# Kernel optimization log

Measured on AMD Instinct MI355X. Metric: run time of the kernel, lower is better.

## Reference

```python
import jax, jax.numpy as jnp
import numpy as np
import math

B, N, D, H, PAIR = 4, 512, 512, 16, 64
DH = D // H

def setup_inputs() -> dict:
    key = jax.random.key(0)
    ks = jax.random.split(key, 8)
    x = jax.random.normal(ks[0], (B, N, D), dtype=jnp.float32)
    pair_bias = jax.random.normal(ks[1], (B, N, N, PAIR), dtype=jnp.float32)
    atom_mask = jax.random.randint(ks[2], (B, N), 0, 2).astype(jnp.bool_)
    s = 1.0 / math.sqrt(D)
    Wq = jax.random.normal(ks[3], (D, D), dtype=jnp.float32) * s
    Wk = jax.random.normal(ks[4], (D, D), dtype=jnp.float32) * s
    Wv = jax.random.normal(ks[5], (D, D), dtype=jnp.float32) * s
    Wo = jax.random.normal(ks[6], (D, D), dtype=jnp.float32) * s
    Wp = jax.random.normal(ks[7], (PAIR, H), dtype=jnp.float32) * (1.0 / math.sqrt(PAIR))
    return {"x": x, "pair_bias": pair_bias, "Wq": Wq, "Wk": Wk, "Wv": Wv,
            "Wo": Wo, "Wp": Wp, "atom_mask": atom_mask}

def reference(x, pair_bias, Wq, Wk, Wv, Wo, Wp, atom_mask):
    b, n, d = x.shape
    # projections -> [B, H, N, DH]
    q = (x @ Wq).reshape(b, n, H, DH).transpose(0, 2, 1, 3)
    k = (x @ Wk).reshape(b, n, H, DH).transpose(0, 2, 1, 3)
    v = (x @ Wv).reshape(b, n, H, DH).transpose(0, 2, 1, 3)
    scores = jnp.einsum('bhnd,bhmd->bhnm', q, k) / math.sqrt(DH)
    # pair bias projected to heads: [B, H, N, N]
    bias = jnp.einsum('bnmp,ph->bhnm', pair_bias, Wp)
    pair_mask = atom_mask[:, :, None] & atom_mask[:, None, :]        # [B, N, N]
    bias = jnp.where(pair_mask[:, None, :, :], bias, 0.0)
    scores = scores + bias
    # key masking with finite large negative, as in the original
    scores = jnp.where(atom_mask[:, None, None, :], scores, jnp.float32(-1e6))
    attn = jax.nn.softmax(scores, axis=-1)
    out = jnp.einsum('bhnm,bhmd->bhnd', attn, v)
    out = out.transpose(0, 2, 1, 3).reshape(b, n, d)
    final = out @ Wo
    final = jnp.where(atom_mask[:, :, None], final, 0.0)
    return (final, attn)
```

## Files before the change

kernel.cpp:

```cpp
#include <hip/hip_runtime.h>

typedef __attribute__((ext_vector_type(8))) short short8;
typedef __attribute__((ext_vector_type(4))) float f32x4;

#define NB 4
#define NN 512
#define ND 512
#define NH 16
#define NDH 32
#define NPAIR 64

static __device__ __forceinline__ unsigned short f2bf(float f) {
    union { float f; unsigned int i; } x; x.f = f;
    unsigned int i = x.i;
    unsigned int r = (i + 0x7fffu + ((i >> 16) & 1u)) >> 16;
    return (unsigned short)r;
}

static __device__ __forceinline__ short8 cvt8(const float4 lo, const float4 hi) {
    short8 r;
    r[0] = (short)f2bf(lo.x); r[1] = (short)f2bf(lo.y);
    r[2] = (short)f2bf(lo.z); r[3] = (short)f2bf(lo.w);
    r[4] = (short)f2bf(hi.x); r[5] = (short)f2bf(hi.y);
    r[6] = (short)f2bf(hi.z); r[7] = (short)f2bf(hi.w);
    return r;
}

__global__ __launch_bounds__(256) void qkv_kernel(
    const float* __restrict__ x, const float* __restrict__ Wq,
    const float* __restrict__ Wk, const float* __restrict__ Wv,
    float* __restrict__ q_ws, float* __restrict__ k_ws, ushort* __restrict__ vT_ws)
{
    __shared__ float xs[8 * 512];
    const int tid = threadIdx.x;
    const int row0 = blockIdx.x * 8;
    const int which = blockIdx.y;
    const float* W = (which == 0) ? Wq : (which == 1) ? Wk : Wv;

    {
        const float4* xg = (const float4*)(x + row0 * 512);
        float4* s = (float4*)xs;
        #pragma unroll
        for (int i = 0; i < 4; ++i) s[tid + i * 256] = xg[tid + i * 256];
    }
    __syncthreads();

    const int c0 = tid * 2;
    float acc[8][2];
    #pragma unroll
    for (int r = 0; r < 8; ++r) { acc[r][0] = 0.f; acc[r][1] = 0.f; }

    for (int kk = 0; kk < 512; kk += 4) {
        float w[4][2];
        #pragma unroll
        for (int j = 0; j < 4; ++j) {
            const float2 u = *(const float2*)(W + (kk + j) * 512 + c0);
            w[j][0] = u.x; w[j][1] = u.y;
        }
        #pragma unroll
        for (int r = 0; r < 8; ++r) {
            const float4 xv = *(const float4*)(xs + r * 512 + kk);
            acc[r][0] = fmaf(xv.x, w[0][0], acc[r][0]);
            acc[r][1] = fmaf(xv.x, w[0][1], acc[r][1]);
            acc[r][0] = fmaf(xv.y, w[1][0], acc[r][0]);
            acc[r][1] = fmaf(xv.y, w[1][1], acc[r][1]);
            acc[r][0] = fmaf(xv.z, w[2][0], acc[r][0]);
            acc[r][1] = fmaf(xv.z, w[2][1], acc[r][1]);
            acc[r][0] = fmaf(xv.w, w[3][0], acc[r][0]);
            acc[r][1] = fmaf(xv.w, w[3][1], acc[r][1]);
        }
    }

    const int h = c0 >> 5, dh = c0 & 31;
    #pragma unroll
    for (int r = 0; r < 8; ++r) {
        int row = row0 + r, b = row >> 9, n = row & 511;
        if (which < 2) {
            float* dst = (which == 0 ? q_ws : k_ws) + (((b * 16 + h) * 512 + n) * 32 + dh);
            *(float2*)dst = make_float2(acc[r][0], acc[r][1]);
        } else {
            ushort* base = vT_ws + ((b * 16 + h) * 32 + dh) * 512 + n;
            base[0]   = f2bf(acc[r][0]);
            base[512] = f2bf(acc[r][1]);
        }
    }
}

__global__ __launch_bounds__(256) void bias_kernel(
    const float* __restrict__ pb, const float* __restrict__ Wp,
    float* __restrict__ bias_out)
{
    const int tid = threadIdx.x;
    const int lane = tid & 63, wid = tid >> 6;
    const int col = lane & 15, quad = lane >> 4;

    short8 b0, b1;
    #pragma unroll
    for (int j = 0; j < 8; ++j) {
        b0[j] = (short)f2bf(Wp[(quad * 8 + j) * 16 + col]);
        b1[j] = (short)f2bf(Wp[(32 + quad * 8 + j) * 16 + col]);
    }

    const int gw = blockIdx.x * 4 + wid;
    #pragma unroll
    for (int i = 0; i < 8; ++i) {
        int tile = gw * 8 + i;
        int mt = tile & 31, n = (tile >> 5) & 511, b = tile >> 14;
        int m0 = mt * 16;
        const float* ap = pb + ((size_t)((b * 512 + n) * 512) + m0 + col) * 64 + quad * 8;
        short8 a0 = cvt8(*(const float4*)(ap),      *(const float4*)(ap + 4));
        short8 a1 = cvt8(*(const float4*)(ap + 32), *(const float4*)(ap + 36));
        f32x4 acc = {0.f, 0.f, 0.f, 0.f};
        acc = __builtin_amdgcn_mfma_f32_16x16x32_bf16(a0, b0, acc, 0, 0, 0);
        acc = __builtin_amdgcn_mfma_f32_16x16x32_bf16(a1, b1, acc, 0, 0, 0);
        float4 o = make_float4(acc[0], acc[1], acc[2], acc[3]);
        *(float4*)(bias_out + ((size_t)(b * 16 + col) * 512 + n) * 512 + m0 + quad * 4) = o;
    }
}

__global__ __launch_bounds__(256) void attn_kernel(
    const float* __restrict__ q_ws, const float* __restrict__ k_ws,
    const int* __restrict__ am, float* __restrict__ attn)
{
    __shared__ float qs[32 * 32];
    __shared__ int amq[32];
    __shared__ float wred[8];
    const int tid = threadIdx.x, lane = tid & 63, wid = tid >> 6;
    const int bh = blockIdx.x >> 4, nt = blockIdx.x & 15;
    const int b = bh >> 4;
    const int n0 = nt * 32;

    {
        const float4* qg = (const float4*)(q_ws + (size_t)(bh * 512 + n0) * 32);
        ((float4*)qs)[tid] = qg[tid];
    }
    if (tid < 32) amq[tid] = am[b * 512 + n0 + tid];

    float k0[32], k1[32];
    {
        const float4* kp  = (const float4*)(k_ws + (size_t)(bh * 512 + tid) * 32);
        const float4* kp2 = (const float4*)(k_ws + (size_t)(bh * 512 + tid + 256) * 32);
        #pragma unroll
        for (int j = 0; j < 8; ++j) {
            float4 u = kp[j];
            k0[j * 4 + 0] = u.x; k0[j * 4 + 1] = u.y; k0[j * 4 + 2] = u.z; k0[j * 4 + 3] = u.w;
            float4 u2 = kp2[j];
            k1[j * 4 + 0] = u2.x; k1[j * 4 + 1] = u2.y; k1[j * 4 + 2] = u2.z; k1[j * 4 + 3] = u2.w;
        }
    }
    const int km0 = am[b * 512 + tid];
    const int km1 = am[b * 512 + 256 + tid];
    __syncthreads();

    const float scale = 0.17677669529663687f;
    float* arow = attn + (size_t)(bh * 512 + n0) * 512;

    for (int r = 0; r < 32; ++r) {
        float s0 = 0.f, s1 = 0.f;
        const float4* q4 = (const float4*)(qs + r * 32);
        #pragma unroll
        for (int j = 0; j < 8; ++j) {
            float4 qv = q4[j];
            s0 = fmaf(qv.x, k0[j * 4 + 0], s0); s1 = fmaf(qv.x, k1[j * 4 + 0], s1);
            s0 = fmaf(qv.y, k0[j * 4 + 1], s0); s1 = fmaf(qv.y, k1[j * 4 + 1], s1);
            s0 = fmaf(qv.z, k0[j * 4 + 2], s0); s1 = fmaf(qv.z, k1[j * 4 + 2], s1);
            s0 = fmaf(qv.w, k0[j * 4 + 3], s0); s1 = fmaf(qv.w, k1[j * 4 + 3], s1);
        }
        float bias0 = arow[r * 512 + tid];
        float bias1 = arow[r * 512 + tid + 256];
        int rm = amq[r];
        s0 = s0 * scale + ((rm && km0) ? bias0 : 0.f);
        s1 = s1 * scale + ((rm && km1) ? bias1 : 0.f);
        if (!km0) s0 = -1e6f;
        if (!km1) s1 = -1e6f;

        float mloc = fmaxf(s0, s1);
        #pragma unroll
        for (int off = 32; off > 0; off >>= 1) mloc = fmaxf(mloc, __shfl_xor(mloc, off));
        if (lane == 0) wred[wid] = mloc;
        __syncthreads();
        float mx = fmaxf(fmaxf(wred[0], wred[1]), fmaxf(wred[2], wred[3]));
        float p0 = __expf(s0 - mx), p1 = __expf(s1 - mx);
        float sl = p0 + p1;
        #pragma unroll
        for (int off = 32; off > 0; off >>= 1) sl += __shfl_xor(sl, off);
        if (lane == 0) wred[4 + wid] = sl;
        __syncthreads();
        float inv = 1.0f / (wred[4] + wred[5] + wred[6] + wred[7]);
        arow[r * 512 + tid]       = p0 * inv;
        arow[r * 512 + tid + 256] = p1 * inv;
        __syncthreads();
    }
}

__global__ __launch_bounds__(256) void av_kernel(
    const float* __restrict__ attn, const ushort* __restrict__ vT,
    float* __restrict__ out_ws)
{
    const int tid = threadIdx.x, lane = tid & 63, wid = tid >> 6;
    const int col = lane & 15, quad = lane >> 4;
    const int wt = blockIdx.x * 4 + wid;
    const int rt = wt & 31, bh = wt >> 5;
    const int n0 = rt * 16;

    const float*  ap  = attn + (size_t)(bh * 512 + n0 + col) * 512 + quad * 8;
    const ushort* vp0 = vT + (size_t)(bh * 32 + col) * 512 + quad * 8;
    const ushort* vp1 = vp0 + 16 * 512;

    f32x4 acc0 = {0.f, 0.f, 0.f, 0.f}, acc1 = {0.f, 0.f, 0.f, 0.f};
    #pragma unroll 4
    for (int kc = 0; kc < 16; ++kc) {
        int mo = kc * 32;
        short8 a  = cvt8(*(const float4*)(ap + mo), *(const float4*)(ap + mo + 4));
        short8 v0 = *(const short8*)(vp0 + mo);
        short8 v1 = *(const short8*)(vp1 + mo);
        acc0 = __builtin_amdgcn_mfma_f32_16x16x32_bf16(a, v0, acc0, 0, 0, 0);
        acc1 = __builtin_amdgcn_mfma_f32_16x16x32_bf16(a, v1, acc1, 0, 0, 0);
    }
    const int b = bh >> 4, h = bh & 15;
    float* op = out_ws + (size_t)(b * 512 + n0 + quad * 4) * 512 + h * 32;
    #pragma unroll
    for (int r = 0; r < 4; ++r) {
        op[r * 512 + col]      = acc0[r];
        op[r * 512 + 16 + col] = acc1[r];
    }
}

__global__ __launch_bounds__(256) void out_kernel(
    const float* __restrict__ out_in, const float* __restrict__ Wo,
    const int* __restrict__ am, float* __restrict__ fin)
{
    __shared__ float xs[8 * 512];
    const int tid = threadIdx.x;
    const int row0 = blockIdx.x * 8;
    {
        const float4* g = (const float4*)(out_in + (size_t)row0 * 512);
        float4* s = (float4*)xs;
        #pragma unroll
        for (int i = 0; i < 4; ++i) s[tid + i * 256] = g[tid + i * 256];
    }
    __syncthreads();

    const int c0 = tid * 2;
    float acc[8][2];
    #pragma unroll
    for (int r = 0; r < 8; ++r) { acc[r][0] = 0.f; acc[r][1] = 0.f; }

    for (int kk = 0; kk < 512; kk += 4) {
        float w[4][2];
        #pragma unroll
        for (int j = 0; j < 4; ++j) {
            const float2 u = *(const float2*)(Wo + (kk + j) * 512 + c0);
            w[j][0] = u.x; w[j][1] = u.y;
        }
        #pragma unroll
        for (int r = 0; r < 8; ++r) {
            const float4 xv = *(const float4*)(xs + r * 512 + kk);
            acc[r][0] = fmaf(xv.x, w[0][0], acc[r][0]);
            acc[r][1] = fmaf(xv.x, w[0][1], acc[r][1]);
            acc[r][0] = fmaf(xv.y, w[1][0], acc[r][0]);
            acc[r][1] = fmaf(xv.y, w[1][1], acc[r][1]);
            acc[r][0] = fmaf(xv.z, w[2][0], acc[r][0]);
            acc[r][1] = fmaf(xv.z, w[2][1], acc[r][1]);
            acc[r][0] = fmaf(xv.w, w[3][0], acc[r][0]);
            acc[r][1] = fmaf(xv.w, w[3][1], acc[r][1]);
        }
    }
    #pragma unroll
    for (int r = 0; r < 8; ++r) {
        int row = row0 + r, b = row >> 9, n = row & 511;
        float msk = am[b * 512 + n] ? 1.0f : 0.0f;
        *(float2*)(fin + (size_t)row * 512 + c0) =
            make_float2(acc[r][0] * msk, acc[r][1] * msk);
    }
}

extern "C" void kernel_launch(void* const* d_in, const int* in_sizes, int n_in,
                              void* d_out, int out_size, void* d_ws, size_t ws_size,
                              hipStream_t stream)
{
    const float* x  = (const float*)d_in[0];
    const float* pb = (const float*)d_in[1];
    const float* Wq = (const float*)d_in[2];
    const float* Wk = (const float*)d_in[3];
    const float* Wv = (const float*)d_in[4];
    const float* Wo = (const float*)d_in[5];
    const float* Wp = (const float*)d_in[6];
    const int*   am = (const int*)d_in[7];

    float* fin  = (float*)d_out;
    float* attn = fin + (size_t)NB * NN * ND;

    float*  q_ws   = (float*)d_ws;
    float*  k_ws   = (float*)((char*)d_ws + 4u * 1024 * 1024);
    ushort* vT     = (ushort*)((char*)d_ws + 8u * 1024 * 1024);
    float*  out_ws = (float*)((char*)d_ws + 10u * 1024 * 1024);

    hipLaunchKernelGGL(qkv_kernel, dim3(256, 3), dim3(256), 0, stream,
                       x, Wq, Wk, Wv, q_ws, k_ws, vT);
    hipLaunchKernelGGL(bias_kernel, dim3(2048), dim3(256), 0, stream,
                       pb, Wp, attn);
    hipLaunchKernelGGL(attn_kernel, dim3(1024), dim3(256), 0, stream,
                       q_ws, k_ws, am, attn);
    hipLaunchKernelGGL(av_kernel, dim3(512), dim3(256), 0, stream,
                       attn, vT, out_ws);
    hipLaunchKernelGGL(out_kernel, dim3(256), dim3(256), 0, stream,
                       out_ws, Wo, am, fin);
}
```

Measured before the change: 601.2 us.

## Fuse softmax with AV matmul, store pair bias as bf16 workspace

The pair-bias projection now writes to a separate bf16 workspace instead of an fp32 staging copy inside the attn output. The softmax kernel and the attention-times-V kernel are merged, so each block computes AV for its 32 rows right after writing them, with the key dimension split across waves and partial sums reduced in shared memory. Double-buffered reduction slots remove one barrier per row. This cuts bias write and read traffic and one kernel launch, and lets the attn re-read hit cache, at the cost of bf16 rounding of the bias and lower AV parallelism per block.

```diff
diff --git a/kernel.cpp b/kernel.cpp
--- a/kernel.cpp
+++ b/kernel.cpp
@@ -10,13 +10,15 @@
 #define NDH 32
 #define NPAIR 64
 
+static __device__ __forceinline__ float bf2f(unsigned short u) {
+    union { unsigned int i; float f; } x; x.i = ((unsigned int)u) << 16; return x.f;
+}
 static __device__ __forceinline__ unsigned short f2bf(float f) {
     union { float f; unsigned int i; } x; x.f = f;
     unsigned int i = x.i;
     unsigned int r = (i + 0x7fffu + ((i >> 16) & 1u)) >> 16;
     return (unsigned short)r;
 }
-
 static __device__ __forceinline__ short8 cvt8(const float4 lo, const float4 hi) {
     short8 r;
     r[0] = (short)f2bf(lo.x); r[1] = (short)f2bf(lo.y);
@@ -88,7 +90,7 @@
 
 __global__ __launch_bounds__(256) void bias_kernel(
     const float* __restrict__ pb, const float* __restrict__ Wp,
-    float* __restrict__ bias_out)
+    ushort* __restrict__ bias_ws)
 {
     const int tid = threadIdx.x;
     const int lane = tid & 63, wid = tid >> 6;
@@ -113,21 +115,25 @@
         f32x4 acc = {0.f, 0.f, 0.f, 0.f};
         acc = __builtin_amdgcn_mfma_f32_16x16x32_bf16(a0, b0, acc, 0, 0, 0);
         acc = __builtin_amdgcn_mfma_f32_16x16x32_bf16(a1, b1, acc, 0, 0, 0);
-        float4 o = make_float4(acc[0], acc[1], acc[2], acc[3]);
-        *(float4*)(bias_out + ((size_t)(b * 16 + col) * 512 + n) * 512 + m0 + quad * 4) = o;
-    }
-}
-
-__global__ __launch_bounds__(256) void attn_kernel(
+        ushort4 o;
+        o.x = f2bf(acc[0]); o.y = f2bf(acc[1]); o.z = f2bf(acc[2]); o.w = f2bf(acc[3]);
+        *(ushort4*)(bias_ws + ((size_t)(b * 16 + col) * 512 + n) * 512 + m0 + quad * 4) = o;
+    }
+}
+
+__global__ __launch_bounds__(256) void attn_av_kernel(
     const float* __restrict__ q_ws, const float* __restrict__ k_ws,
-    const int* __restrict__ am, float* __restrict__ attn)
+    const ushort* __restrict__ bias_ws, const ushort* __restrict__ vT,
+    const int* __restrict__ am, float* __restrict__ attn,
+    float* __restrict__ out_ws)
 {
     __shared__ float qs[32 * 32];
     __shared__ int amq[32];
-    __shared__ float wred[8];
+    __shared__ float wred[2][2][4];
+    __shared__ float red[4 * 528];
     const int tid = threadIdx.x, lane = tid & 63, wid = tid >> 6;
     const int bh = blockIdx.x >> 4, nt = blockIdx.x & 15;
-    const int b = bh >> 4;
+    const int b = bh >> 4, h = bh & 15;
     const int n0 = nt * 32;
 
     {
@@ -154,6 +160,7 @@
 
     const float scale = 0.17677669529663687f;
     float* arow = attn + (size_t)(bh * 512 + n0) * 512;
+    const ushort* brow = bias_ws + (size_t)(bh * 512 + n0) * 512;
 
     for (int r = 0; r < 32; ++r) {
         float s0 = 0.f, s1 = 0.f;
@@ -166,50 +173,45 @@
             s0 = fmaf(qv.z, k0[j * 4 + 2], s0); s1 = fmaf(qv.z, k1[j * 4 + 2], s1);
             s0 = fmaf(qv.w, k0[j * 4 + 3], s0); s1 = fmaf(qv.w, k1[j * 4 + 3], s1);
         }
-        float bias0 = arow[r * 512 + tid];
-        float bias1 = arow[r * 512 + tid + 256];
+        float bias0 = bf2f(brow[r * 512 + tid]);
+        float bias1 = bf2f(brow[r * 512 + tid + 256]);
         int rm = amq[r];
         s0 = s0 * scale + ((rm && km0) ? bias0 : 0.f);
         s1 = s1 * scale + ((rm && km1) ? bias1 : 0.f);
         if (!km0) s0 = -1e6f;
         if (!km1) s1 = -1e6f;
 
+        const int par = r & 1;
         float mloc = fmaxf(s0, s1);
         #pragma unroll
         for (int off = 32; off > 0; off >>= 1) mloc = fmaxf(mloc, __shfl_xor(mloc, off));
-        if (lane == 0) wred[wid] = mloc;
+        if (lane == 0) wred[par][0][wid] = mloc;
         __syncthreads();
-        float mx = fmaxf(fmaxf(wred[0], wred[1]), fmaxf(wred[2], wred[3]));
+        float mx = fmaxf(fmaxf(wred[par][0][0], wred[par][0][1]),
+                         fmaxf(wred[par][0][2], wred[par][0][3]));
         float p0 = __expf(s0 - mx), p1 = __expf(s1 - mx);
         float sl = p0 + p1;
         #pragma unroll
         for (int off = 32; off > 0; off >>= 1) sl += __shfl_xor(sl, off);
-        if (lane == 0) wred[4 + wid] = sl;
+        if (lane == 0) wred[par][1][wid] = sl;
         __syncthreads();
-        float inv = 1.0f / (wred[4] + wred[5] + wred[6] + wred[7]);
+        float inv = 1.0f / (wred[par][1][0] + wred[par][1][1] +
+                            wred[par][1][2] + wred[par][1][3]);
         arow[r * 512 + tid]       = p0 * inv;
         arow[r * 512 + tid + 256] = p1 * inv;
-        __syncthreads();
-    }
-}
-
-__global__ __launch_bounds__(256) void av_kernel(
-    const float* __restrict__ attn, const ushort* __restrict__ vT,
-    float* __restrict__ out_ws)
-{
-    const int tid = threadIdx.x, lane = tid & 63, wid = tid >> 6;
+    }
+
+    __syncthreads();
     const int col = lane & 15, quad = lane >> 4;
-    const int wt = blockIdx.x * 4 + wid;
-    const int rt = wt & 31, bh = wt >> 5;
-    const int n0 = rt * 16;
-
-    const float*  ap  = attn + (size_t)(bh * 512 + n0 + col) * 512 + quad * 8;
-    const ushort* vp0 = vT + (size_t)(bh * 32 + col) * 512 + quad * 8;
+    const int t = wid & 1, kh = wid >> 1;
+
+    const float*  ap  = attn + (size_t)(bh * 512 + n0 + t * 16 + col) * 512 + kh * 256 + quad * 8;
+    const ushort* vp0 = vT + (size_t)(bh * 32 + col) * 512 + kh * 256 + quad * 8;
     const ushort* vp1 = vp0 + 16 * 512;
 
     f32x4 acc0 = {0.f, 0.f, 0.f, 0.f}, acc1 = {0.f, 0.f, 0.f, 0.f};
-    #pragma unroll 4
-    for (int kc = 0; kc < 16; ++kc) {
+    #pragma unroll
+    for (int kc = 0; kc < 8; ++kc) {
         int mo = kc * 32;
         short8 a  = cvt8(*(const float4*)(ap + mo), *(const float4*)(ap + mo + 4));
         short8 v0 = *(const short8*)(vp0 + mo);
@@ -217,12 +219,25 @@
         acc0 = __builtin_amdgcn_mfma_f32_16x16x32_bf16(a, v0, acc0, 0, 0, 0);
         acc1 = __builtin_amdgcn_mfma_f32_16x16x32_bf16(a, v1, acc1, 0, 0, 0);
     }
-    const int b = bh >> 4, h = bh & 15;
-    float* op = out_ws + (size_t)(b * 512 + n0 + quad * 4) * 512 + h * 32;
-    #pragma unroll
-    for (int r = 0; r < 4; ++r) {
-        op[r * 512 + col]      = acc0[r];
-        op[r * 512 + 16 + col] = acc1[r];
+    {
+        float* my = red + wid * 528;
+        #pragma unroll
+        for (int r = 0; r < 4; ++r) {
+            my[(quad * 4 + r) * 33 + col]      = acc0[r];
+            my[(quad * 4 + r) * 33 + 16 + col] = acc1[r];
+        }
+    }
+    __syncthreads();
+    if (wid < 2) {
+        const float* r0 = red + wid * 528;
+        const float* r1 = red + (2 + wid) * 528;
+        float* op = out_ws + (size_t)(b * 512 + n0 + wid * 16 + quad * 4) * 512 + h * 32;
+        #pragma unroll
+        for (int r = 0; r < 4; ++r) {
+            int i0 = (quad * 4 + r) * 33 + col;
+            op[r * 512 + col]      = r0[i0] + r1[i0];
+            op[r * 512 + 16 + col] = r0[i0 + 16] + r1[i0 + 16];
+        }
     }
 }
 
@@ -291,19 +306,18 @@
     float* fin  = (float*)d_out;
     float* attn = fin + (size_t)NB * NN * ND;
 
-    float*  q_ws   = (float*)d_ws;
-    float*  k_ws   = (float*)((char*)d_ws + 4u * 1024 * 1024);
-    ushort* vT     = (ushort*)((char*)d_ws + 8u * 1024 * 1024);
-    float*  out_ws = (float*)((char*)d_ws + 10u * 1024 * 1024);
+    float*  q_ws    = (float*)d_ws;
+    float*  k_ws    = (float*)((char*)d_ws + 4u * 1024 * 1024);
+    ushort* vT      = (ushort*)((char*)d_ws + 8u * 1024 * 1024);
+    float*  out_ws  = (float*)((char*)d_ws + 10u * 1024 * 1024);
+    ushort* bias_ws = (ushort*)((char*)d_ws + 14u * 1024 * 1024);
 
     hipLaunchKernelGGL(qkv_kernel, dim3(256, 3), dim3(256), 0, stream,
                        x, Wq, Wk, Wv, q_ws, k_ws, vT);
     hipLaunchKernelGGL(bias_kernel, dim3(2048), dim3(256), 0, stream,
-                       pb, Wp, attn);
-    hipLaunchKernelGGL(attn_kernel, dim3(1024), dim3(256), 0, stream,
-                       q_ws, k_ws, am, attn);
-    hipLaunchKernelGGL(av_kernel, dim3(512), dim3(256), 0, stream,
-                       attn, vT, out_ws);
+                       pb, Wp, bias_ws);
+    hipLaunchKernelGGL(attn_av_kernel, dim3(1024), dim3(256), 0, stream,
+                       q_ws, k_ws, bias_ws, vT, am, attn, out_ws);
     hipLaunchKernelGGL(out_kernel, dim3(256), dim3(256), 0, stream,
                        out_ws, Wo, am, fin);
 }
```

New measurement: 594.9 us. Within noise of the previous version (-1.0%).
